# Performance work log

Hardware: AMD Instinct MI355X
Metric: run time of the kernel (lower is better)

The kernel has to match this reference:

```python
import jax, jax.numpy as jnp
import numpy as np
from jax import lax

B, C, H, W = 16, 256, 64, 64
KNUM, KS, STRIDE, PAD, RED, GROUPS = 4, 3, 1, 1, 16, 4
BN_EPS = 1e-5


def setup_inputs() -> dict:
    key = jax.random.key(0)
    ks = jax.random.split(key, 12)
    f = jax.random.normal
    half, red = C // 2, C // RED
    return {
        "x": f(ks[0], (B, C, H, W), jnp.float32),
        "att_conv1d_w": f(ks[1], (3,), jnp.float32) * 0.5,                      # shared Conv1d(1,1,3) in Attention
        "att_out_w": f(ks[2], (C, C), jnp.float32) * (2.0 / C) ** 0.5,          # out_channel_conv2d 1x1
        "att_kernel_w": f(ks[3], (KNUM, C), jnp.float32) * (2.0 / C) ** 0.5,    # kernel_conv2d 1x1
        "ede_weight": f(ks[4], (KNUM, C, C, KS, KS), jnp.float32) * (2.0 / (C * KS * KS)) ** 0.5,
        "lga_conv1d_w": f(ks[5], (3,), jnp.float32) * 0.5,                      # LGA Conv1d(1,1,3) with bias
        "lga_conv1d_b": f(ks[6], (1,), jnp.float32) * 0.1,
        "lga_mlp_w1": f(ks[7], (red, half), jnp.float32) * (2.0 / half) ** 0.5,  # mlp conv 1x1 (no bias)
        "lga_mlp_w2": f(ks[8], (half, red), jnp.float32) * (2.0 / red) ** 0.5,
        "bn_gamma": jnp.ones((C,), jnp.float32),
        "bn_beta": jnp.zeros((C,), jnp.float32),
    }


def _conv1d_same(v_bc, w3):
    # 1-channel cross-correlation along the channel axis, pad=1 (PyTorch Conv1d)
    y = lax.conv_general_dilated(v_bc[:, None, :], w3[None, None, :], (1,), [(1, 1)],
                                 dimension_numbers=("NCH", "OIH", "NCH"))
    return y[:, 0, :]


def reference(x, att_conv1d_w, att_out_w, att_kernel_w, ede_weight,
              lga_conv1d_w, lga_conv1d_b, lga_mlp_w1, lga_mlp_w2,
              bn_gamma, bn_beta):
    b, c, h, w = x.shape

    # ---- EDE (Q branch): dynamic per-sample conv ----
    gap = x.mean(axis=(2, 3))                              # (b, c) global avg pool
    t = _conv1d_same(gap, att_conv1d_w)                    # shared conv1d over channels
    in_att = jax.nn.sigmoid(t)[:, :, None, None]           # (b, c, 1, 1)
    out_att = jax.nn.sigmoid(t @ att_out_w.T)[:, :, None, None]
    k_att = jax.nn.softmax(t @ att_kernel_w.T, axis=1)     # (b, KNUM)
    agg_w = jnp.einsum("bk,koipq->boipq", k_att, ede_weight)  # (b, C, C, KS, KS)
    x_mod = x * in_att

    def per_sample(xi, wi):  # xi: (C,H,W), wi: (C,C,KS,KS)
        return lax.conv_general_dilated(xi[None], wi, (STRIDE, STRIDE),
                                        [(PAD, PAD), (PAD, PAD)])[0]

    Q = jax.vmap(per_sample)(x_mod, agg_w) * out_att       # (b, C, H, W)

    # ---- LGA (K branch) ----
    half = c // 2
    in1, in2 = x[:, :half], x[:, half:]
    s = _conv1d_same(in1.mean(axis=(2, 3)), lga_conv1d_w) + lga_conv1d_b
    x1 = in1 * jax.nn.sigmoid(s)[:, :, None, None]

    def mlp(v):  # (b, half) -> (b, half); 1x1 convs on (b,half,1,1) == matmuls
        return jax.nn.relu(v @ lga_mlp_w1.T) @ lga_mlp_w2.T

    ch = jax.nn.sigmoid(mlp(in2.max(axis=(2, 3))) + mlp(in2.mean(axis=(2, 3))))
    y2 = in2 * ch[:, :, None, None]
    K = jnp.concatenate([x1, y2], axis=1)
    # channel shuffle with GROUPS groups
    K = K.reshape(b, GROUPS, c // GROUPS, h, w).transpose(0, 2, 1, 3, 4).reshape(b, c, h, w)

    # ---- fuse + BatchNorm (training-mode batch stats) + ReLU ----
    z = Q + K
    mean = z.mean(axis=(0, 2, 3))
    var = z.var(axis=(0, 2, 3))
    zn = (z - mean[None, :, None, None]) * lax.rsqrt(var[None, :, None, None] + BN_EPS)
    return jax.nn.relu(zn * bn_gamma[None, :, None, None] + bn_beta[None, :, None, None])
```

## Files before the change

kernel.cpp:

```cpp
#include <hip/hip_runtime.h>
#include <hip/hip_bf16.h>
#include <stdint.h>

#define HW_ 4096

typedef float f32x4 __attribute__((ext_vector_type(4)));
typedef short bf16x8 __attribute__((ext_vector_type(8)));

__device__ __forceinline__ unsigned short f2bf(float f) {
  __hip_bfloat16 h = __float2bfloat16(f);
  return *reinterpret_cast<unsigned short*>(&h);
}
__device__ __forceinline__ float sigmoidf_(float x) { return 1.f / (1.f + __expf(-x)); }

__device__ __forceinline__ void glds16(const void* g, void* l) {
  __builtin_amdgcn_global_load_lds(
      (const __attribute__((address_space(1))) unsigned int*)g,
      (__attribute__((address_space(3))) unsigned int*)l, 16, 0, 0);
}

__global__ void k_pre(const float* __restrict__ x, unsigned short* __restrict__ xtr,
                      float* __restrict__ psum, float* __restrict__ pmax) {
  int hwb = blockIdx.x;
  int cb = blockIdx.y;
  int b = blockIdx.z;
  int t = threadIdx.x;
  __shared__ float sv[64][65];
  int h16 = t & 15, g = t >> 4;
#pragma unroll
  for (int i = 0; i < 4; ++i) {
    int c_l = g + i * 16;
    float4 v = *reinterpret_cast<const float4*>(
        x + (((size_t)b * 256 + cb * 64 + c_l) << 12) + hwb * 64 + h16 * 4);
    *reinterpret_cast<float4*>(&sv[c_l][h16 * 4]) = v;
  }
  __syncthreads();
  {
    int c_l = t >> 2, q = t & 3;
    float s16 = 0.f, m16 = -3.4e38f;
#pragma unroll
    for (int j = 0; j < 16; ++j) {
      float vv = sv[c_l][q * 16 + j];
      s16 += vv; m16 = fmaxf(m16, vv);
    }
    s16 += __shfl_xor(s16, 1); s16 += __shfl_xor(s16, 2);
    m16 = fmaxf(m16, __shfl_xor(m16, 1)); m16 = fmaxf(m16, __shfl_xor(m16, 2));
    if (q == 0) {
      int c = cb * 64 + c_l;
      psum[(((size_t)b * 256 + c) << 6) + hwb] = s16;
      pmax[(((size_t)b * 256 + c) << 6) + hwb] = m16;
    }
  }
#pragma unroll
  for (int i = 0; i < 2; ++i) {
    int fp = t + i * 256;
    int hw2 = fp >> 3;
    int cp = (fp & 7) * 8;
    uint4 uu;
    uu.x = (unsigned)f2bf(sv[cp + 0][hw2]) | ((unsigned)f2bf(sv[cp + 1][hw2]) << 16);
    uu.y = (unsigned)f2bf(sv[cp + 2][hw2]) | ((unsigned)f2bf(sv[cp + 3][hw2]) << 16);
    uu.z = (unsigned)f2bf(sv[cp + 4][hw2]) | ((unsigned)f2bf(sv[cp + 5][hw2]) << 16);
    uu.w = (unsigned)f2bf(sv[cp + 6][hw2]) | ((unsigned)f2bf(sv[cp + 7][hw2]) << 16);
    *reinterpret_cast<uint4*>(xtr + (((size_t)b * 4096 + hwb * 64 + hw2) << 8) + cb * 64 + cp) = uu;
  }
}

__global__ void k_tiny(const float* __restrict__ psum, const float* __restrict__ pmax,
                       const float* __restrict__ aw3, const float* __restrict__ Wout,
                       const float* __restrict__ Wk, const float* __restrict__ lw3,
                       const float* __restrict__ lbia, const float* __restrict__ mw1,
                       const float* __restrict__ mw2,
                       float* __restrict__ in_att, float* __restrict__ out_att,
                       float* __restrict__ katt, float* __restrict__ sc,
                       float* __restrict__ sums, float* __restrict__ zerop) {
  int b = blockIdx.x, t = threadIdx.x;
  __shared__ float g[256], tt[256], red[256], hsum[16], ksm[4], mx[128];
  {
    const float4* pp = reinterpret_cast<const float4*>(psum + ((size_t)(b * 256 + t) << 6));
    const float4* pm = reinterpret_cast<const float4*>(pmax + ((size_t)(b * 256 + t) << 6));
    float s = 0.f, m = -3.4e38f;
#pragma unroll
    for (int j = 0; j < 16; ++j) {
      float4 a = pp[j]; s += (a.x + a.y) + (a.z + a.w);
      float4 q4 = pm[j];
      m = fmaxf(m, fmaxf(fmaxf(q4.x, q4.y), fmaxf(q4.z, q4.w)));
    }
    g[t] = s * (1.f / 4096.f);
    if (t >= 128) mx[t - 128] = m;
  }
  if (b == 0) {
    sums[t] = 0.f; sums[256 + t] = 0.f;
    zerop[t] = 0.f;
  }
  __syncthreads();
  float c0 = aw3[0], c1 = aw3[1], c2 = aw3[2];
  float tv = c1 * g[t];
  if (t > 0) tv += c0 * g[t - 1];
  if (t < 255) tv += c2 * g[t + 1];
  tt[t] = tv;
  in_att[b * 256 + t] = sigmoidf_(tv);
  __syncthreads();
  {
    float d = 0.f;
    const float4* wr = reinterpret_cast<const float4*>(Wout + (size_t)t * 256);
    for (int c4 = 0; c4 < 64; ++c4) {
      float4 wv4 = wr[c4];
      d += tt[c4 * 4] * wv4.x + tt[c4 * 4 + 1] * wv4.y + tt[c4 * 4 + 2] * wv4.z + tt[c4 * 4 + 3] * wv4.w;
    }
    out_att[b * 256 + t] = sigmoidf_(d);
  }
  int k = t >> 6, lane = t & 63;
  {
    float pk = 0.f;
    for (int c = lane; c < 256; c += 64) pk += tt[c] * Wk[k * 256 + c];
    red[t] = pk; __syncthreads();
    for (int off = 32; off > 0; off >>= 1) {
      if (lane < off) red[t] += red[t + off];
      __syncthreads();
    }
    if (t == 0) {
      float l0 = red[0], l1 = red[64], l2 = red[128], l3 = red[192];
      float mm = fmaxf(fmaxf(l0, l1), fmaxf(l2, l3));
      float e0 = __expf(l0 - mm), e1 = __expf(l1 - mm), e2 = __expf(l2 - mm), e3 = __expf(l3 - mm);
      float inv = 1.f / (e0 + e1 + e2 + e3);
      ksm[0] = e0 * inv; ksm[1] = e1 * inv; ksm[2] = e2 * inv; ksm[3] = e3 * inv;
    }
    __syncthreads();
    if (t < 4) katt[b * 4 + t] = ksm[t];
  }
  if (t < 128) {
    float a0 = lw3[0], a1 = lw3[1], a2 = lw3[2];
    float sv = a1 * g[t] + lbia[0];
    if (t > 0) sv += a0 * g[t - 1];
    if (t < 127) sv += a2 * g[t + 1];
    sc[b * 256 + t] = sigmoidf_(sv);
  }
  __syncthreads();
  if (t < 16) {
    float d1 = 0.f, d2 = 0.f;
    const float* w1r = mw1 + t * 128;
    for (int j = 0; j < 128; ++j) { d1 += mx[j] * w1r[j]; d2 += g[128 + j] * w1r[j]; }
    hsum[t] = fmaxf(d1, 0.f) + fmaxf(d2, 0.f);
  }
  __syncthreads();
  if (t < 128) {
    float dd = 0.f;
    const float* w2r = mw2 + t * 16;
    for (int r = 0; r < 16; ++r) dd += hsum[r] * w2r[r];
    sc[b * 256 + 128 + t] = sigmoidf_(dd);
  }
}

__global__ __launch_bounds__(256) void k_agg(const float* __restrict__ ede,
                                             const float* __restrict__ katt,
                                             const float* __restrict__ inatt,
                                             unsigned short* __restrict__ agg) {
  __shared__ float eds[4][2304];
  int o = blockIdx.x, t = threadIdx.x;
#pragma unroll
  for (int k = 0; k < 4; ++k) {
    const float* src = ede + ((size_t)k * 256 + o) * 2304;
#pragma unroll
    for (int j = 0; j < 9; ++j) eds[k][j * 256 + t] = src[j * 256 + t];
  }
  __syncthreads();
  int ii = (t & 127) * 2;
  int bh = t >> 7;
  int fg = o >> 4, r = o & 15;
  int cs = ii >> 5, lh = (ii >> 3) & 3, jj = ii & 7;
  for (int b2 = 0; b2 < 8; ++b2) {
    int b = b2 * 2 + bh;
    float k0 = katt[b * 4], k1 = katt[b * 4 + 1], k2 = katt[b * 4 + 2], k3 = katt[b * 4 + 3];
    float ia0 = inatt[b * 256 + ii], ia1 = inatt[b * 256 + ii + 1];
#pragma unroll
    for (int pq = 0; pq < 9; ++pq) {
      float v0 = k0 * eds[0][ii * 9 + pq] + k1 * eds[1][ii * 9 + pq] +
                 k2 * eds[2][ii * 9 + pq] + k3 * eds[3][ii * 9 + pq];
      float v1 = k0 * eds[0][(ii + 1) * 9 + pq] + k1 * eds[1][(ii + 1) * 9 + pq] +
                 k2 * eds[2][(ii + 1) * 9 + pq] + k3 * eds[3][(ii + 1) * 9 + pq];
      v0 *= ia0; v1 *= ia1;
      unsigned int u = (unsigned)f2bf(v0) | ((unsigned)f2bf(v1) << 16);
      size_t base = (((((size_t)(b * 9 + pq) * 8 + cs) * 16 + fg) * 64 + lh * 16 + r) << 3) + jj;
      *reinterpret_cast<unsigned int*>(agg + base) = u;
    }
  }
}

__global__ __launch_bounds__(512, 2) void k_conv(
    const unsigned short* __restrict__ agg, const unsigned short* __restrict__ xtr,
    const float* __restrict__ x, const float* __restrict__ oatt,
    const float* __restrict__ sc, const float* __restrict__ zerop,
    float* __restrict__ sums, float* __restrict__ zout) {
  __shared__ __align__(16) char smem[49152];
  int wg = blockIdx.x;
  int bswz = ((wg & 7) << 5) | (wg >> 3);
  int b = bswz >> 4, pt = bswz & 15;
  int tid = threadIdx.x;
  int l = tid & 63;
  int wv = tid >> 6;
  int wm = wv >> 2, wn = wv & 3;
  int w0 = l & 15, ks = l >> 4;
  bool maskl0 = (w0 == 0), maskl15 = (w0 == 15);

  auto slabsrc = [&](int j) -> const char* {
    int idx = j * 512 + tid;
    int P = idx >> 2, sp = idx & 3;
    int sr = P >> 6, w = P & 63;
    int imgrow = pt * 4 + sr - 1;
    int ir = imgrow < 0 ? 0 : (imgrow > 63 ? 63 : imgrow);
    int slog = sp ^ ((w >> 1) & 3);
    const char* gp = (const char*)(xtr + (((size_t)b * 4096 + ir * 64 + w) << 8) + slog * 8);
    return ((unsigned)imgrow < 64u) ? gp : (const char*)zerop;
  };
  const char* sb0_ = slabsrc(0);
  const char* sb1_ = slabsrc(1);
  const char* sb2_ = slabsrc(2);

  auto aP = [&](int pq, int cs, int fm) -> const unsigned short* {
    return agg + (((((size_t)(b * 9 + pq) * 8 + cs) * 16 + wm * 8 + fm) << 9)) + l * 8;
  };

  f32x4 acc[8][4];
  f32x4 zero4 = {0.f, 0.f, 0.f, 0.f};
#pragma unroll
  for (int i2 = 0; i2 < 8; ++i2)
#pragma unroll
    for (int j2 = 0; j2 < 4; ++j2) acc[i2][j2] = zero4;

  bf16x8 z8 = {0, 0, 0, 0, 0, 0, 0, 0};
  bf16x8 af[8], afn[8];

  {
    char* sd = smem;
    glds16(sb0_, sd + tid * 16);
    glds16(sb1_, sd + 8192 + tid * 16);
    glds16(sb2_, sd + 16384 + tid * 16);
  }
#pragma unroll
  for (int fm = 0; fm < 8; ++fm) af[fm] = *reinterpret_cast<const bf16x8*>(aP(0, 0, fm));
  asm volatile("s_waitcnt vmcnt(0)" ::: "memory");
  __builtin_amdgcn_s_barrier();

  for (int c = 0; c < 8; ++c) {
    const char* sb = smem + ((c & 1) ? 24576 : 0);
    if (c < 7) {
      char* sd = smem + (((c + 1) & 1) ? 24576 : 0);
      glds16(sb0_ + (c + 1) * 64, sd + tid * 16);
      glds16(sb1_ + (c + 1) * 64, sd + 8192 + tid * 16);
      glds16(sb2_ + (c + 1) * 64, sd + 16384 + tid * 16);
    }
    int cn = (c < 7) ? c + 1 : 7;
#pragma unroll
    for (int pq = 0; pq < 9; ++pq) {
      const int dp = pq / 3, dq = pq % 3;
      {
        const int npq = (pq < 8) ? pq + 1 : 0;
        int ncs = (pq < 8) ? c : cn;
#pragma unroll
        for (int fm = 0; fm < 8; ++fm)
          afn[fm] = *reinterpret_cast<const bf16x8*>(aP(npq, ncs, fm));
      }
      bf16x8 bv[4];
      int rowb = (wn + dp) << 6;
#pragma unroll
      for (int fn = 0; fn < 4; ++fn) {
        int wcol = w0 + fn * 16 + (dq - 1);
        int wc = wcol < 0 ? 0 : (wcol > 63 ? 63 : wcol);
        int bo = ((rowb + wc) << 6) + ((ks ^ ((wc >> 1) & 3)) << 4);
        bv[fn] = *reinterpret_cast<const bf16x8*>(sb + bo);
      }
      if (dq == 0) bv[0] = maskl0 ? z8 : bv[0];
      if (dq == 2) bv[3] = maskl15 ? z8 : bv[3];
      __builtin_amdgcn_s_setprio(1);
#pragma unroll
      for (int fm = 0; fm < 8; ++fm)
#pragma unroll
        for (int fn = 0; fn < 4; ++fn)
          acc[fm][fn] = __builtin_amdgcn_mfma_f32_16x16x32_bf16(af[fm], bv[fn], acc[fm][fn], 0, 0, 0);
      __builtin_amdgcn_s_setprio(0);
#pragma unroll
      for (int fm = 0; fm < 8; ++fm) af[fm] = afn[fm];
    }
    asm volatile("s_waitcnt vmcnt(0)" ::: "memory");
    __builtin_amdgcn_s_barrier();
  }
  __syncthreads();

  float* ls = (float*)smem;
  ls[tid] = 0.f;
  __syncthreads();

#pragma unroll
  for (int fm = 0; fm < 8; ++fm) {
#pragma unroll
    for (int r = 0; r < 4; ++r) {
      int m = wm * 128 + fm * 16 + ((l >> 4) << 2) + r;
      int oc = ((m & 3) << 6) | (m >> 2);
      float oav = oatt[b * 256 + m];
      float scv = sc[b * 256 + oc];
      const float* xrow = x + (((size_t)b * 256 + oc) << 12) + pt * 256;
      float* zrow = zout + (((size_t)b * 256 + m) << 12) + pt * 256;
      float psv = 0.f, psv2 = 0.f;
#pragma unroll
      for (int fn = 0; fn < 4; ++fn) {
        int n = wn * 64 + fn * 16 + (l & 15);
        float zv = acc[fm][fn][r] * oav + xrow[n] * scv;
        zrow[n] = zv;
        psv += zv; psv2 += zv * zv;
      }
#pragma unroll
      for (int d = 8; d > 0; d >>= 1) {
        psv += __shfl_down(psv, d, 16);
        psv2 += __shfl_down(psv2, d, 16);
      }
      if ((l & 15) == 0) {
        atomicAdd(&ls[m], psv);
        atomicAdd(&ls[256 + m], psv2);
      }
    }
  }
  __syncthreads();
  if (tid < 256) {
    atomicAdd(&sums[tid], ls[tid]);
    atomicAdd(&sums[256 + tid], ls[256 + tid]);
  }
}

__global__ void k_apply(float* __restrict__ z, const float* __restrict__ sums,
                        const float* __restrict__ gamma, const float* __restrict__ beta) {
  int idx = blockIdx.x * 256 + threadIdx.x;
  for (int i = idx; i < 4194304; i += 4096 * 256) {
    int c = (i >> 10) & 255;
    float mean = sums[c] * (1.f / 65536.f);
    float var = sums[256 + c] * (1.f / 65536.f) - mean * mean;
    float scale = gamma[c] * rsqrtf(var + 1e-5f);
    float shift = beta[c] - mean * scale;
    float4* p = reinterpret_cast<float4*>(z) + i;
    float4 v = *p;
    v.x = fmaxf(v.x * scale + shift, 0.f);
    v.y = fmaxf(v.y * scale + shift, 0.f);
    v.z = fmaxf(v.z * scale + shift, 0.f);
    v.w = fmaxf(v.w * scale + shift, 0.f);
    *p = v;
  }
}

extern "C" void kernel_launch(void* const* d_in, const int* in_sizes, int n_in,
                              void* d_out, int out_size, void* d_ws, size_t ws_size,
                              hipStream_t stream) {
  (void)in_sizes; (void)n_in; (void)out_size; (void)ws_size;
  const float* x = (const float*)d_in[0];
  const float* aw3 = (const float*)d_in[1];
  const float* Wout = (const float*)d_in[2];
  const float* Wk = (const float*)d_in[3];
  const float* ede = (const float*)d_in[4];
  const float* lw3 = (const float*)d_in[5];
  const float* lbia = (const float*)d_in[6];
  const float* mw1 = (const float*)d_in[7];
  const float* mw2 = (const float*)d_in[8];
  const float* gamma = (const float*)d_in[9];
  const float* beta = (const float*)d_in[10];

  char* ws = (char*)d_ws;
  float* inatt = (float*)(ws + 32768);
  float* oatt  = (float*)(ws + 49152);
  float* katt  = (float*)(ws + 65536);
  float* sc    = (float*)(ws + 65792);
  float* zerop = (float*)(ws + 82176);
  float* sums  = (float*)(ws + 83200);
  unsigned short* xtr = (unsigned short*)(ws + 262144);
  unsigned short* agg = (unsigned short*)(ws + 262144 + 33554432);
  float* psum = (float*)(ws + 262144 + 33554432);
  float* pmax = (float*)(ws + 262144 + 33554432 + 1048576);
  float* z = (float*)d_out;

  k_pre<<<dim3(64, 4, 16), 256, 0, stream>>>(x, xtr, psum, pmax);
  k_tiny<<<16, 256, 0, stream>>>(psum, pmax, aw3, Wout, Wk, lw3, lbia, mw1, mw2,
                                 inatt, oatt, katt, sc, sums, zerop);
  k_agg<<<256, 256, 0, stream>>>(ede, katt, inatt, agg);
  k_conv<<<256, 512, 0, stream>>>(agg, xtr, x, oatt, sc, zerop, sums, z);
  k_apply<<<4096, 256, 0, stream>>>(z, sums, gamma, beta);
}
```

Before: 161.0 us.

## Split conv output channels across two workgroups and drop A-fragment prefetch

The conv kernel now launches 512 workgroups instead of 256, with each workgroup computing half of the output channels (128). Accumulators shrink from 8x4 to 4x4 fragments and launch bounds ask for 4 waves-per-EU occupancy, so more workgroups can share the 256 CUs. The software prefetch of the next weight fragments is removed and weights are loaded directly each tap. In exchange, every input slab is loaded twice and weight-load latency is no longer hidden by prefetch.

```diff
diff --git a/kernel.cpp b/kernel.cpp
--- a/kernel.cpp
+++ b/kernel.cpp
@@ -186,15 +186,17 @@
   }
 }
 
-__global__ __launch_bounds__(512, 2) void k_conv(
+__global__ __launch_bounds__(512, 4) void k_conv(
     const unsigned short* __restrict__ agg, const unsigned short* __restrict__ xtr,
     const float* __restrict__ x, const float* __restrict__ oatt,
     const float* __restrict__ sc, const float* __restrict__ zerop,
     float* __restrict__ sums, float* __restrict__ zout) {
   __shared__ __align__(16) char smem[49152];
   int wg = blockIdx.x;
-  int bswz = ((wg & 7) << 5) | (wg >> 3);
-  int b = bswz >> 4, pt = bswz & 15;
+  int bswz = ((wg & 7) << 6) | (wg >> 3);
+  int b = bswz >> 5;
+  int ot = (bswz >> 4) & 1;
+  int pt = bswz & 15;
   int tid = threadIdx.x;
   int l = tid & 63;
   int wv = tid >> 6;
@@ -217,18 +219,17 @@
   const char* sb2_ = slabsrc(2);
 
   auto aP = [&](int pq, int cs, int fm) -> const unsigned short* {
-    return agg + (((((size_t)(b * 9 + pq) * 8 + cs) * 16 + wm * 8 + fm) << 9)) + l * 8;
+    return agg + ((((size_t)(b * 9 + pq) * 8 + cs) * 16 + ot * 8 + wm * 4 + fm) << 9) + l * 8;
   };
 
-  f32x4 acc[8][4];
+  f32x4 acc[4][4];
   f32x4 zero4 = {0.f, 0.f, 0.f, 0.f};
 #pragma unroll
-  for (int i2 = 0; i2 < 8; ++i2)
+  for (int i2 = 0; i2 < 4; ++i2)
 #pragma unroll
     for (int j2 = 0; j2 < 4; ++j2) acc[i2][j2] = zero4;
 
   bf16x8 z8 = {0, 0, 0, 0, 0, 0, 0, 0};
-  bf16x8 af[8], afn[8];
 
   {
     char* sd = smem;
@@ -236,8 +237,6 @@
     glds16(sb1_, sd + 8192 + tid * 16);
     glds16(sb2_, sd + 16384 + tid * 16);
   }
-#pragma unroll
-  for (int fm = 0; fm < 8; ++fm) af[fm] = *reinterpret_cast<const bf16x8*>(aP(0, 0, fm));
   asm volatile("s_waitcnt vmcnt(0)" ::: "memory");
   __builtin_amdgcn_s_barrier();
 
@@ -249,17 +248,13 @@
       glds16(sb1_ + (c + 1) * 64, sd + 8192 + tid * 16);
       glds16(sb2_ + (c + 1) * 64, sd + 16384 + tid * 16);
     }
-    int cn = (c < 7) ? c + 1 : 7;
 #pragma unroll
     for (int pq = 0; pq < 9; ++pq) {
       const int dp = pq / 3, dq = pq % 3;
-      {
-        const int npq = (pq < 8) ? pq + 1 : 0;
-        int ncs = (pq < 8) ? c : cn;
-#pragma unroll
-        for (int fm = 0; fm < 8; ++fm)
-          afn[fm] = *reinterpret_cast<const bf16x8*>(aP(npq, ncs, fm));
-      }
+      bf16x8 af[4];
+#pragma unroll
+      for (int fm = 0; fm < 4; ++fm)
+        af[fm] = *reinterpret_cast<const bf16x8*>(aP(pq, c, fm));
       bf16x8 bv[4];
       int rowb = (wn + dp) << 6;
 #pragma unroll
@@ -273,13 +268,11 @@
       if (dq == 2) bv[3] = maskl15 ? z8 : bv[3];
       __builtin_amdgcn_s_setprio(1);
 #pragma unroll
-      for (int fm = 0; fm < 8; ++fm)
+      for (int fm = 0; fm < 4; ++fm)
 #pragma unroll
         for (int fn = 0; fn < 4; ++fn)
           acc[fm][fn] = __builtin_amdgcn_mfma_f32_16x16x32_bf16(af[fm], bv[fn], acc[fm][fn], 0, 0, 0);
       __builtin_amdgcn_s_setprio(0);
-#pragma unroll
-      for (int fm = 0; fm < 8; ++fm) af[fm] = afn[fm];
     }
     asm volatile("s_waitcnt vmcnt(0)" ::: "memory");
     __builtin_amdgcn_s_barrier();
@@ -287,19 +280,20 @@
   __syncthreads();
 
   float* ls = (float*)smem;
-  ls[tid] = 0.f;
-  __syncthreads();
-
-#pragma unroll
-  for (int fm = 0; fm < 8; ++fm) {
+  if (tid < 256) ls[tid] = 0.f;
+  __syncthreads();
+
+#pragma unroll
+  for (int fm = 0; fm < 4; ++fm) {
 #pragma unroll
     for (int r = 0; r < 4; ++r) {
-      int m = wm * 128 + fm * 16 + ((l >> 4) << 2) + r;
-      int oc = ((m & 3) << 6) | (m >> 2);
-      float oav = oatt[b * 256 + m];
+      int ml = wm * 64 + fm * 16 + ((l >> 4) << 2) + r;
+      int gm = ot * 128 + ml;
+      int oc = ((gm & 3) << 6) | (gm >> 2);
+      float oav = oatt[b * 256 + gm];
       float scv = sc[b * 256 + oc];
       const float* xrow = x + (((size_t)b * 256 + oc) << 12) + pt * 256;
-      float* zrow = zout + (((size_t)b * 256 + m) << 12) + pt * 256;
+      float* zrow = zout + (((size_t)b * 256 + gm) << 12) + pt * 256;
       float psv = 0.f, psv2 = 0.f;
 #pragma unroll
       for (int fn = 0; fn < 4; ++fn) {
@@ -314,15 +308,15 @@
         psv2 += __shfl_down(psv2, d, 16);
       }
       if ((l & 15) == 0) {
-        atomicAdd(&ls[m], psv);
-        atomicAdd(&ls[256 + m], psv2);
+        atomicAdd(&ls[ml], psv);
+        atomicAdd(&ls[128 + ml], psv2);
       }
     }
   }
   __syncthreads();
-  if (tid < 256) {
-    atomicAdd(&sums[tid], ls[tid]);
-    atomicAdd(&sums[256 + tid], ls[256 + tid]);
+  if (tid < 128) {
+    atomicAdd(&sums[ot * 128 + tid], ls[tid]);
+    atomicAdd(&sums[256 + ot * 128 + tid], ls[128 + tid]);
   }
 }
 
@@ -378,6 +372,6 @@
   k_tiny<<<16, 256, 0, stream>>>(psum, pmax, aw3, Wout, Wk, lw3, lbia, mw1, mw2,
                                  inatt, oatt, katt, sc, sums, zerop);
   k_agg<<<256, 256, 0, stream>>>(ede, katt, inatt, agg);
-  k_conv<<<256, 512, 0, stream>>>(agg, xtr, x, oatt, sc, zerop, sums, z);
+  k_conv<<<512, 512, 0, stream>>>(agg, xtr, x, oatt, sc, zerop, sums, z);
   k_apply<<<4096, 256, 0, stream>>>(z, sums, gamma, beta);
 }
```

Measured after the change: 156.5 us. 1.03x faster.
